# Performance work log

Hardware: AMD Instinct MI355X
Metric: run time of the kernel (lower is better)

## Reference

```python
import jax, jax.numpy as jnp
import numpy as np

M, B, T, DIN, H, E, NEMB = 6, 128, 32, 64, 512, 512, 32


def setup_inputs() -> dict:
    key = jax.random.key(0)
    ks = jax.random.split(key, 6)
    return {
        "state_btD": jax.random.normal(ks[0], (B, T, M * DIN), dtype=jnp.float32),
        "emb_ids": jax.random.randint(ks[1], (B,), 0, NEMB),
        # stacked per-modality, per-embodiment adapter params (all modalities share dims)
        "W1": 0.02 * jax.random.normal(ks[2], (M, NEMB, DIN, H), dtype=jnp.float32),
        "b1": jnp.zeros((M, NEMB, H), dtype=jnp.float32),
        "W2": 0.02 * jax.random.normal(ks[3], (M, NEMB, H, E), dtype=jnp.float32),
        "b2": jnp.zeros((M, NEMB, E), dtype=jnp.float32),
        "type_embed": 0.02 * jax.random.normal(ks[4], (M, E), dtype=jnp.float32),
    }


def reference(state_btD, emb_ids, W1, b1, W2, b2, type_embed):
    Bb, Tt, _ = state_btD.shape
    # slices are contiguous equal-size chunks -> (B, T, M, DIN)
    x = state_btD.reshape(Bb, Tt, M, DIN)
    # layer1: per-sample gathered weights W1[:, emb_ids] -> (M, B, DIN, H)
    h = jax.nn.relu(
        jnp.einsum('btmi,mbih->btmh', x, W1[:, emb_ids])
        + b1[:, emb_ids].transpose(1, 0, 2)[:, None]  # (B,1,M,H)
    )
    # layer2 + type embed
    z = (
        jnp.einsum('btmh,mbho->btmo', h, W2[:, emb_ids])
        + b2[:, emb_ids].transpose(1, 0, 2)[:, None]
        + type_embed[None, None]  # (1,1,M,E)
    )
    # torch.cat(tokens, dim=1): modality-major along the token axis -> (B, M*T, E)
    return z.transpose(0, 2, 1, 3).reshape(Bb, M * Tt, E)
```

## Files before the change

### kernel.cpp

```cpp
#include <hip/hip_runtime.h>

#define MM   6
#define BB   128
#define TT   32
#define DIN  64
#define HH   512
#define EE   512
#define NEMB 32
#define XP   72
#define HP   520

typedef __attribute__((ext_vector_type(8))) short bf16x8;
typedef __attribute__((ext_vector_type(4))) float f32x4;

static __device__ __forceinline__ unsigned short f2bf(float f) {
    unsigned int u = __float_as_uint(f);
    u += 0x7FFFu + ((u >> 16) & 1u);
    return (unsigned short)(u >> 16);
}
static __device__ __forceinline__ float bf2f(unsigned short h) {
    return __uint_as_float(((unsigned int)h) << 16);
}


__global__ __launch_bounds__(256, 2) void tok_mfma(
    const float* __restrict__ state,
    const int*   __restrict__ emb_ids,
    const float* __restrict__ W1,
    const float* __restrict__ b1,
    const float* __restrict__ W2,
    const float* __restrict__ b2,
    const float* __restrict__ te,
    float* __restrict__ out)
{
    __shared__ __align__(16) unsigned short x_hi[TT][XP];
    __shared__ __align__(16) unsigned short x_lo[TT][XP];
    __shared__ __align__(16) unsigned short h_hi[TT][HP];
    __shared__ __align__(16) unsigned short h_lo[TT][HP];

    const int tid  = threadIdx.x;
    const int lane = tid & 63;
    const int w    = tid >> 6;
    const int lr   = lane & 15;
    const int lg   = lane >> 4;

    const int bm = blockIdx.x;
    const int m  = bm % MM;
    const int b  = bm / MM;
    const int id = emb_ids[b];

    const float* xg  = state + (size_t)b * TT * (MM * DIN) + m * DIN;
    const float* W1p = W1 + (size_t)(m * NEMB + id) * DIN * HH;
    const float* b1p = b1 + (size_t)(m * NEMB + id) * HH;
    const float* W2p = W2 + (size_t)(m * NEMB + id) * HH * EE;
    const float* b2p = b2 + (size_t)(m * NEMB + id) * EE;
    const float* tep = te + m * EE;

    #pragma unroll
    for (int k = 0; k < 2; ++k) {
        int f  = k * 256 + tid;
        int t  = f >> 4;
        int i4 = f & 15;
        float4 v = *reinterpret_cast<const float4*>(xg + (size_t)t * (MM * DIN) + i4 * 4);
        ushort4 hi, lo;
        hi.x = f2bf(v.x); lo.x = f2bf(v.x - bf2f(hi.x));
        hi.y = f2bf(v.y); lo.y = f2bf(v.y - bf2f(hi.y));
        hi.z = f2bf(v.z); lo.z = f2bf(v.z - bf2f(hi.z));
        hi.w = f2bf(v.w); lo.w = f2bf(v.w - bf2f(hi.w));
        *reinterpret_cast<ushort4*>(&x_hi[t][i4 * 4]) = hi;
        *reinterpret_cast<ushort4*>(&x_lo[t][i4 * 4]) = lo;
    }
    __syncthreads();

    bf16x8 xa_h[2][2], xa_l[2][2];
    #pragma unroll
    for (int r0 = 0; r0 < 2; ++r0)
        #pragma unroll
        for (int kk = 0; kk < 2; ++kk) {
            xa_h[r0][kk] = *reinterpret_cast<const bf16x8*>(&x_hi[r0 * 16 + lr][kk * 32 + lg * 8]);
            xa_l[r0][kk] = *reinterpret_cast<const bf16x8*>(&x_lo[r0 * 16 + lr][kk * 32 + lg * 8]);
        }

    #pragma unroll
    for (int j = 0; j < 8; ++j) {
        const int n = w * 128 + j * 16 + lr;
        float bv = b1p[n];
        f32x4 a0 = {bv, bv, bv, bv};
        f32x4 a1 = {bv, bv, bv, bv};
        #pragma unroll
        for (int kk = 0; kk < 2; ++kk) {
            const float* wp = W1p + (size_t)(kk * 32 + lg * 8) * HH + n;
            bf16x8 bh, bl;
            #pragma unroll
            for (int i = 0; i < 8; ++i) {
                float wv = wp[(size_t)i * HH];
                unsigned short h_ = f2bf(wv);
                bh[i] = (short)h_;
                bl[i] = (short)f2bf(wv - bf2f(h_));
            }
            a0 = __builtin_amdgcn_mfma_f32_16x16x32_bf16(xa_h[0][kk], bh, a0, 0, 0, 0);
            a0 = __builtin_amdgcn_mfma_f32_16x16x32_bf16(xa_h[0][kk], bl, a0, 0, 0, 0);
            a0 = __builtin_amdgcn_mfma_f32_16x16x32_bf16(xa_l[0][kk], bh, a0, 0, 0, 0);
            a1 = __builtin_amdgcn_mfma_f32_16x16x32_bf16(xa_h[1][kk], bh, a1, 0, 0, 0);
            a1 = __builtin_amdgcn_mfma_f32_16x16x32_bf16(xa_h[1][kk], bl, a1, 0, 0, 0);
            a1 = __builtin_amdgcn_mfma_f32_16x16x32_bf16(xa_l[1][kk], bh, a1, 0, 0, 0);
        }
        #pragma unroll
        for (int r = 0; r < 4; ++r) {
            float h0 = fmaxf(a0[r], 0.0f);
            unsigned short hh0 = f2bf(h0);
            h_hi[lg * 4 + r][n] = hh0;
            h_lo[lg * 4 + r][n] = f2bf(h0 - bf2f(hh0));
            float h1 = fmaxf(a1[r], 0.0f);
            unsigned short hh1 = f2bf(h1);
            h_hi[16 + lg * 4 + r][n] = hh1;
            h_lo[16 + lg * 4 + r][n] = f2bf(h1 - bf2f(hh1));
        }
    }
    __syncthreads();

    float bias2[8];
    #pragma unroll
    for (int j = 0; j < 8; ++j) {
        int n = w * 128 + j * 16 + lr;
        bias2[j] = b2p[n] + tep[n];
    }
    f32x4 acc[2][8];
    #pragma unroll
    for (int r0 = 0; r0 < 2; ++r0)
        #pragma unroll
        for (int j = 0; j < 8; ++j) {
            f32x4 t0 = {bias2[j], bias2[j], bias2[j], bias2[j]};
            acc[r0][j] = t0;
        }

    for (int kk = 0; kk < 16; ++kk) {
        bf16x8 ah0 = *reinterpret_cast<const bf16x8*>(&h_hi[lr][kk * 32 + lg * 8]);
        bf16x8 al0 = *reinterpret_cast<const bf16x8*>(&h_lo[lr][kk * 32 + lg * 8]);
        bf16x8 ah1 = *reinterpret_cast<const bf16x8*>(&h_hi[16 + lr][kk * 32 + lg * 8]);
        bf16x8 al1 = *reinterpret_cast<const bf16x8*>(&h_lo[16 + lr][kk * 32 + lg * 8]);
        #pragma unroll
        for (int j = 0; j < 8; ++j) {
            const float* wp = W2p + (size_t)(kk * 32 + lg * 8) * EE + (w * 128 + j * 16 + lr);
            bf16x8 bh, bl;
            #pragma unroll
            for (int i = 0; i < 8; ++i) {
                float wv = wp[(size_t)i * EE];
                unsigned short h_ = f2bf(wv);
                bh[i] = (short)h_;
                bl[i] = (short)f2bf(wv - bf2f(h_));
            }
            acc[0][j] = __builtin_amdgcn_mfma_f32_16x16x32_bf16(ah0, bh, acc[0][j], 0, 0, 0);
            acc[0][j] = __builtin_amdgcn_mfma_f32_16x16x32_bf16(ah0, bl, acc[0][j], 0, 0, 0);
            acc[0][j] = __builtin_amdgcn_mfma_f32_16x16x32_bf16(al0, bh, acc[0][j], 0, 0, 0);
            acc[1][j] = __builtin_amdgcn_mfma_f32_16x16x32_bf16(ah1, bh, acc[1][j], 0, 0, 0);
            acc[1][j] = __builtin_amdgcn_mfma_f32_16x16x32_bf16(ah1, bl, acc[1][j], 0, 0, 0);
            acc[1][j] = __builtin_amdgcn_mfma_f32_16x16x32_bf16(al1, bh, acc[1][j], 0, 0, 0);
        }
    }

    float* outp = out + ((size_t)(b * MM + m) * TT) * EE;
    #pragma unroll
    for (int r0 = 0; r0 < 2; ++r0)
        #pragma unroll
        for (int j = 0; j < 8; ++j) {
            int n = w * 128 + j * 16 + lr;
            #pragma unroll
            for (int r = 0; r < 4; ++r) {
                int row = r0 * 16 + lg * 4 + r;
                outp[(size_t)row * EE + n] = acc[r0][j][r];
            }
        }
}

extern "C" void kernel_launch(void* const* d_in, const int* in_sizes, int n_in,
                              void* d_out, int out_size, void* d_ws, size_t ws_size,
                              hipStream_t stream) {
    const float* state   = (const float*)d_in[0];
    const int*   emb_ids = (const int*)d_in[1];
    const float* W1      = (const float*)d_in[2];
    const float* b1      = (const float*)d_in[3];
    const float* W2      = (const float*)d_in[4];
    const float* b2      = (const float*)d_in[5];
    const float* te      = (const float*)d_in[6];
    float*       out     = (float*)d_out;

    dim3 grid(BB * MM);
    dim3 block(256);
    tok_mfma<<<grid, block, 0, stream>>>(state, emb_ids, W1, b1, W2, b2, te, out);
}
```

Measured before the change: 372.7 us.

## Bucket samples by embodiment and process two samples per block to share weights

```diff
diff --git a/kernel.cpp b/kernel.cpp
--- a/kernel.cpp
+++ b/kernel.cpp
@@ -9,6 +9,8 @@
 #define NEMB 32
 #define XP   72
 #define HP   520
+#define ROWS 64
+#define MAXCH 64
 
 typedef __attribute__((ext_vector_type(8))) short bf16x8;
 typedef __attribute__((ext_vector_type(4))) float f32x4;
@@ -22,10 +24,22 @@
     return __uint_as_float(((unsigned int)h) << 16);
 }
 
-
-__global__ __launch_bounds__(256, 2) void tok_mfma(
+__global__ void bucket_k(const int* __restrict__ emb_ids,
+                         int* __restrict__ cnt, int* __restrict__ lists) {
+    int t = threadIdx.x;
+    if (t < NEMB) cnt[t] = 0;
+    __syncthreads();
+    if (t < BB) {
+        int id = emb_ids[t];
+        int slot = atomicAdd(&cnt[id], 1);
+        lists[id * BB + slot] = t;
+    }
+}
+
+__global__ __launch_bounds__(512, 2) void tok_mfma2(
     const float* __restrict__ state,
-    const int*   __restrict__ emb_ids,
+    const int*   __restrict__ cnt,
+    const int*   __restrict__ lists,
     const float* __restrict__ W1,
     const float* __restrict__ b1,
     const float* __restrict__ W2,
@@ -33,10 +47,19 @@
     const float* __restrict__ te,
     float* __restrict__ out)
 {
-    __shared__ __align__(16) unsigned short x_hi[TT][XP];
-    __shared__ __align__(16) unsigned short x_lo[TT][XP];
-    __shared__ __align__(16) unsigned short h_hi[TT][HP];
-    __shared__ __align__(16) unsigned short h_lo[TT][HP];
+    __shared__ __align__(16) unsigned short x_hi[ROWS][XP];
+    __shared__ __align__(16) unsigned short x_lo[ROWS][XP];
+    __shared__ __align__(16) unsigned short h_hi[ROWS][HP];
+    __shared__ __align__(16) unsigned short h_lo[ROWS][HP];
+
+    const int c  = blockIdx.x;
+    const int id = blockIdx.y;
+    const int m  = blockIdx.z;
+    const int n_b = cnt[id];
+    if (c * 2 >= n_b) return;
+    const int nb  = (n_b - c * 2 >= 2) ? 2 : 1;
+    const int ba0 = lists[id * BB + c * 2];
+    const int ba1 = lists[id * BB + c * 2 + (nb - 1)];
 
     const int tid  = threadIdx.x;
     const int lane = tid & 63;
@@ -44,12 +67,6 @@
     const int lr   = lane & 15;
     const int lg   = lane >> 4;
 
-    const int bm = blockIdx.x;
-    const int m  = bm % MM;
-    const int b  = bm / MM;
-    const int id = emb_ids[b];
-
-    const float* xg  = state + (size_t)b * TT * (MM * DIN) + m * DIN;
     const float* W1p = W1 + (size_t)(m * NEMB + id) * DIN * HH;
     const float* b1p = b1 + (size_t)(m * NEMB + id) * HH;
     const float* W2p = W2 + (size_t)(m * NEMB + id) * HH * EE;
@@ -57,36 +74,39 @@
     const float* tep = te + m * EE;
 
     #pragma unroll
-    for (int k = 0; k < 2; ++k) {
-        int f  = k * 256 + tid;
-        int t  = f >> 4;
+    for (int kq = 0; kq < 2; ++kq) {
+        int f  = kq * 512 + tid;
+        int r  = f >> 4;
         int i4 = f & 15;
-        float4 v = *reinterpret_cast<const float4*>(xg + (size_t)t * (MM * DIN) + i4 * 4);
+        int bsel = (r < 32) ? ba0 : ba1;
+        const float* xg = state + ((size_t)bsel * TT + (r & 31)) * (MM * DIN) + m * DIN + i4 * 4;
+        float4 v = *reinterpret_cast<const float4*>(xg);
         ushort4 hi, lo;
         hi.x = f2bf(v.x); lo.x = f2bf(v.x - bf2f(hi.x));
         hi.y = f2bf(v.y); lo.y = f2bf(v.y - bf2f(hi.y));
         hi.z = f2bf(v.z); lo.z = f2bf(v.z - bf2f(hi.z));
         hi.w = f2bf(v.w); lo.w = f2bf(v.w - bf2f(hi.w));
-        *reinterpret_cast<ushort4*>(&x_hi[t][i4 * 4]) = hi;
-        *reinterpret_cast<ushort4*>(&x_lo[t][i4 * 4]) = lo;
+        *reinterpret_cast<ushort4*>(&x_hi[r][i4 * 4]) = hi;
+        *reinterpret_cast<ushort4*>(&x_lo[r][i4 * 4]) = lo;
     }
     __syncthreads();
 
-    bf16x8 xa_h[2][2], xa_l[2][2];
-    #pragma unroll
-    for (int r0 = 0; r0 < 2; ++r0)
+    bf16x8 xa_h[4][2], xa_l[4][2];
+    #pragma unroll
+    for (int rt = 0; rt < 4; ++rt)
         #pragma unroll
         for (int kk = 0; kk < 2; ++kk) {
-            xa_h[r0][kk] = *reinterpret_cast<const bf16x8*>(&x_hi[r0 * 16 + lr][kk * 32 + lg * 8]);
-            xa_l[r0][kk] = *reinterpret_cast<const bf16x8*>(&x_lo[r0 * 16 + lr][kk * 32 + lg * 8]);
-        }
-
-    #pragma unroll
-    for (int j = 0; j < 8; ++j) {
-        const int n = w * 128 + j * 16 + lr;
+            xa_h[rt][kk] = *reinterpret_cast<const bf16x8*>(&x_hi[rt * 16 + lr][kk * 32 + lg * 8]);
+            xa_l[rt][kk] = *reinterpret_cast<const bf16x8*>(&x_lo[rt * 16 + lr][kk * 32 + lg * 8]);
+        }
+
+    #pragma unroll
+    for (int j = 0; j < 4; ++j) {
+        const int n = w * 64 + j * 16 + lr;
         float bv = b1p[n];
-        f32x4 a0 = {bv, bv, bv, bv};
-        f32x4 a1 = {bv, bv, bv, bv};
+        f32x4 a[4];
+        #pragma unroll
+        for (int rt = 0; rt < 4; ++rt) { f32x4 t0 = {bv, bv, bv, bv}; a[rt] = t0; }
         #pragma unroll
         for (int kk = 0; kk < 2; ++kk) {
             const float* wp = W1p + (size_t)(kk * 32 + lg * 8) * HH + n;
@@ -98,50 +118,50 @@
                 bh[i] = (short)h_;
                 bl[i] = (short)f2bf(wv - bf2f(h_));
             }
-            a0 = __builtin_amdgcn_mfma_f32_16x16x32_bf16(xa_h[0][kk], bh, a0, 0, 0, 0);
-            a0 = __builtin_amdgcn_mfma_f32_16x16x32_bf16(xa_h[0][kk], bl, a0, 0, 0, 0);
-            a0 = __builtin_amdgcn_mfma_f32_16x16x32_bf16(xa_l[0][kk], bh, a0, 0, 0, 0);
-            a1 = __builtin_amdgcn_mfma_f32_16x16x32_bf16(xa_h[1][kk], bh, a1, 0, 0, 0);
-            a1 = __builtin_amdgcn_mfma_f32_16x16x32_bf16(xa_h[1][kk], bl, a1, 0, 0, 0);
-            a1 = __builtin_amdgcn_mfma_f32_16x16x32_bf16(xa_l[1][kk], bh, a1, 0, 0, 0);
-        }
-        #pragma unroll
-        for (int r = 0; r < 4; ++r) {
-            float h0 = fmaxf(a0[r], 0.0f);
-            unsigned short hh0 = f2bf(h0);
-            h_hi[lg * 4 + r][n] = hh0;
-            h_lo[lg * 4 + r][n] = f2bf(h0 - bf2f(hh0));
-            float h1 = fmaxf(a1[r], 0.0f);
-            unsigned short hh1 = f2bf(h1);
-            h_hi[16 + lg * 4 + r][n] = hh1;
-            h_lo[16 + lg * 4 + r][n] = f2bf(h1 - bf2f(hh1));
-        }
+            #pragma unroll
+            for (int rt = 0; rt < 4; ++rt) {
+                a[rt] = __builtin_amdgcn_mfma_f32_16x16x32_bf16(xa_h[rt][kk], bh, a[rt], 0, 0, 0);
+                a[rt] = __builtin_amdgcn_mfma_f32_16x16x32_bf16(xa_h[rt][kk], bl, a[rt], 0, 0, 0);
+                a[rt] = __builtin_amdgcn_mfma_f32_16x16x32_bf16(xa_l[rt][kk], bh, a[rt], 0, 0, 0);
+            }
+        }
+        #pragma unroll
+        for (int rt = 0; rt < 4; ++rt)
+            #pragma unroll
+            for (int r = 0; r < 4; ++r) {
+                float hv = fmaxf(a[rt][r], 0.0f);
+                unsigned short hh = f2bf(hv);
+                h_hi[rt * 16 + lg * 4 + r][n] = hh;
+                h_lo[rt * 16 + lg * 4 + r][n] = f2bf(hv - bf2f(hh));
+            }
     }
     __syncthreads();
 
-    float bias2[8];
-    #pragma unroll
-    for (int j = 0; j < 8; ++j) {
-        int n = w * 128 + j * 16 + lr;
+    float bias2[4];
+    #pragma unroll
+    for (int j = 0; j < 4; ++j) {
+        int n = w * 64 + j * 16 + lr;
         bias2[j] = b2p[n] + tep[n];
     }
-    f32x4 acc[2][8];
-    #pragma unroll
-    for (int r0 = 0; r0 < 2; ++r0)
-        #pragma unroll
-        for (int j = 0; j < 8; ++j) {
+    f32x4 acc[4][4];
+    #pragma unroll
+    for (int rt = 0; rt < 4; ++rt)
+        #pragma unroll
+        for (int j = 0; j < 4; ++j) {
             f32x4 t0 = {bias2[j], bias2[j], bias2[j], bias2[j]};
-            acc[r0][j] = t0;
+            acc[rt][j] = t0;
         }
 
     for (int kk = 0; kk < 16; ++kk) {
-        bf16x8 ah0 = *reinterpret_cast<const bf16x8*>(&h_hi[lr][kk * 32 + lg * 8]);
-        bf16x8 al0 = *reinterpret_cast<const bf16x8*>(&h_lo[lr][kk * 32 + lg * 8]);
-        bf16x8 ah1 = *reinterpret_cast<const bf16x8*>(&h_hi[16 + lr][kk * 32 + lg * 8]);
-        bf16x8 al1 = *reinterpret_cast<const bf16x8*>(&h_lo[16 + lr][kk * 32 + lg * 8]);
-        #pragma unroll
-        for (int j = 0; j < 8; ++j) {
-            const float* wp = W2p + (size_t)(kk * 32 + lg * 8) * EE + (w * 128 + j * 16 + lr);
+        bf16x8 ah[4], al[4];
+        #pragma unroll
+        for (int rt = 0; rt < 4; ++rt) {
+            ah[rt] = *reinterpret_cast<const bf16x8*>(&h_hi[rt * 16 + lr][kk * 32 + lg * 8]);
+            al[rt] = *reinterpret_cast<const bf16x8*>(&h_lo[rt * 16 + lr][kk * 32 + lg * 8]);
+        }
+        #pragma unroll
+        for (int j = 0; j < 4; ++j) {
+            const float* wp = W2p + (size_t)(kk * 32 + lg * 8) * EE + (w * 64 + j * 16 + lr);
             bf16x8 bh, bl;
             #pragma unroll
             for (int i = 0; i < 8; ++i) {
@@ -150,27 +170,29 @@
                 bh[i] = (short)h_;
                 bl[i] = (short)f2bf(wv - bf2f(h_));
             }
-            acc[0][j] = __builtin_amdgcn_mfma_f32_16x16x32_bf16(ah0, bh, acc[0][j], 0, 0, 0);
-            acc[0][j] = __builtin_amdgcn_mfma_f32_16x16x32_bf16(ah0, bl, acc[0][j], 0, 0, 0);
-            acc[0][j] = __builtin_amdgcn_mfma_f32_16x16x32_bf16(al0, bh, acc[0][j], 0, 0, 0);
-            acc[1][j] = __builtin_amdgcn_mfma_f32_16x16x32_bf16(ah1, bh, acc[1][j], 0, 0, 0);
-            acc[1][j] = __builtin_amdgcn_mfma_f32_16x16x32_bf16(ah1, bl, acc[1][j], 0, 0, 0);
-            acc[1][j] = __builtin_amdgcn_mfma_f32_16x16x32_bf16(al1, bh, acc[1][j], 0, 0, 0);
-        }
-    }
-
-    float* outp = out + ((size_t)(b * MM + m) * TT) * EE;
-    #pragma unroll
-    for (int r0 = 0; r0 < 2; ++r0)
-        #pragma unroll
-        for (int j = 0; j < 8; ++j) {
-            int n = w * 128 + j * 16 + lr;
-            #pragma unroll
-            for (int r = 0; r < 4; ++r) {
-                int row = r0 * 16 + lg * 4 + r;
-                outp[(size_t)row * EE + n] = acc[r0][j][r];
-            }
-        }
+            #pragma unroll
+            for (int rt = 0; rt < 4; ++rt) {
+                acc[rt][j] = __builtin_amdgcn_mfma_f32_16x16x32_bf16(ah[rt], bh, acc[rt][j], 0, 0, 0);
+                acc[rt][j] = __builtin_amdgcn_mfma_f32_16x16x32_bf16(ah[rt], bl, acc[rt][j], 0, 0, 0);
+                acc[rt][j] = __builtin_amdgcn_mfma_f32_16x16x32_bf16(al[rt], bh, acc[rt][j], 0, 0, 0);
+            }
+        }
+    }
+
+    #pragma unroll
+    for (int rt = 0; rt < 4; ++rt) {
+        int bi = rt >> 1;
+        if (bi >= nb) continue;
+        int bglob = (bi == 0) ? ba0 : ba1;
+        float* outp = out + (((size_t)bglob * MM + m) * TT + (rt & 1) * 16 + lg * 4) * EE;
+        #pragma unroll
+        for (int j = 0; j < 4; ++j) {
+            int n = w * 64 + j * 16 + lr;
+            #pragma unroll
+            for (int r = 0; r < 4; ++r)
+                outp[(size_t)r * EE + n] = acc[rt][j][r];
+        }
+    }
 }
 
 extern "C" void kernel_launch(void* const* d_in, const int* in_sizes, int n_in,
@@ -185,7 +207,10 @@
     const float* te      = (const float*)d_in[6];
     float*       out     = (float*)d_out;
 
-    dim3 grid(BB * MM);
-    dim3 block(256);
-    tok_mfma<<<grid, block, 0, stream>>>(state, emb_ids, W1, b1, W2, b2, te, out);
-}
+    int* cnt   = (int*)d_ws;
+    int* lists = cnt + NEMB;
+
+    bucket_k<<<dim3(1), dim3(128), 0, stream>>>(emb_ids, cnt, lists);
+    tok_mfma2<<<dim3(MAXCH, NEMB, MM), dim3(512), 0, stream>>>(
+        state, cnt, lists, W1, b1, W2, b2, te, out);
+}
```

Result: slower. 1.039 ms (+178.9%).

## Group blocks by embodiment for L2 reuse and stage W2 loads through LDS

Applied to the files above, without the earlier changes.

```diff
diff --git a/kernel.cpp b/kernel.cpp
--- a/kernel.cpp
+++ b/kernel.cpp
@@ -9,6 +9,7 @@
 #define NEMB 32
 #define XP   72
 #define HP   520
+#define TRS  36
 
 typedef __attribute__((ext_vector_type(8))) short bf16x8;
 typedef __attribute__((ext_vector_type(4))) float f32x4;
@@ -22,21 +23,42 @@
     return __uint_as_float(((unsigned int)h) << 16);
 }
 
-
-__global__ __launch_bounds__(256, 2) void tok_mfma(
+__global__ void order_k(const int* __restrict__ emb_ids, int* __restrict__ ent) {
+    __shared__ int cnt_s[NEMB], psum_s[NEMB], slot_s[BB], id_s[BB];
+    int t = threadIdx.x;
+    if (t < NEMB) cnt_s[t] = 0;
+    __syncthreads();
+    if (t < BB) { int id = emb_ids[t]; id_s[t] = id; slot_s[t] = atomicAdd(&cnt_s[id], 1); }
+    __syncthreads();
+    if (t == 0) { int r = 0; for (int i = 0; i < NEMB; ++i) { psum_s[i] = r; r += cnt_s[i]; } }
+    __syncthreads();
+    if (t < BB) {
+        int id = id_s[t], sl = slot_s[t], base = psum_s[id] * MM, c = cnt_s[id];
+        for (int mm = 0; mm < MM; ++mm) ent[base + mm * c + sl] = (t << 3) | mm;
+    }
+}
+
+__global__ __launch_bounds__(256, 2) void tok_mfma4(
     const float* __restrict__ state,
-    const int*   __restrict__ emb_ids,
+    const int*   __restrict__ ent,
     const float* __restrict__ W1,
     const float* __restrict__ b1,
     const float* __restrict__ W2,
     const float* __restrict__ b2,
     const float* __restrict__ te,
+    const int*   __restrict__ emb_ids,
     float* __restrict__ out)
 {
-    __shared__ __align__(16) unsigned short x_hi[TT][XP];
-    __shared__ __align__(16) unsigned short x_lo[TT][XP];
+    __shared__ __align__(16) unsigned char regA[10240];
     __shared__ __align__(16) unsigned short h_hi[TT][HP];
     __shared__ __align__(16) unsigned short h_lo[TT][HP];
+
+    const int bid = blockIdx.x;
+    const int s   = (bid & 7) * 96 + (bid >> 3);
+    const int e   = ent[s];
+    const int b   = e >> 3;
+    const int m   = e & 7;
+    const int id  = emb_ids[b];
 
     const int tid  = threadIdx.x;
     const int lane = tid & 63;
@@ -44,21 +66,19 @@
     const int lr   = lane & 15;
     const int lg   = lane >> 4;
 
-    const int bm = blockIdx.x;
-    const int m  = bm % MM;
-    const int b  = bm / MM;
-    const int id = emb_ids[b];
-
-    const float* xg  = state + (size_t)b * TT * (MM * DIN) + m * DIN;
     const float* W1p = W1 + (size_t)(m * NEMB + id) * DIN * HH;
     const float* b1p = b1 + (size_t)(m * NEMB + id) * HH;
     const float* W2p = W2 + (size_t)(m * NEMB + id) * HH * EE;
     const float* b2p = b2 + (size_t)(m * NEMB + id) * EE;
     const float* tep = te + m * EE;
-
-    #pragma unroll
-    for (int k = 0; k < 2; ++k) {
-        int f  = k * 256 + tid;
+    const float* xg  = state + (size_t)b * TT * (MM * DIN) + m * DIN;
+
+    unsigned short (*x_hi)[XP] = (unsigned short(*)[XP])regA;
+    unsigned short (*x_lo)[XP] = (unsigned short(*)[XP])(regA + 4608);
+
+    #pragma unroll
+    for (int kq = 0; kq < 2; ++kq) {
+        int f  = kq * 256 + tid;
         int t  = f >> 4;
         int i4 = f & 15;
         float4 v = *reinterpret_cast<const float4*>(xg + (size_t)t * (MM * DIN) + i4 * 4);
@@ -74,11 +94,11 @@
 
     bf16x8 xa_h[2][2], xa_l[2][2];
     #pragma unroll
-    for (int r0 = 0; r0 < 2; ++r0)
+    for (int rt = 0; rt < 2; ++rt)
         #pragma unroll
         for (int kk = 0; kk < 2; ++kk) {
-            xa_h[r0][kk] = *reinterpret_cast<const bf16x8*>(&x_hi[r0 * 16 + lr][kk * 32 + lg * 8]);
-            xa_l[r0][kk] = *reinterpret_cast<const bf16x8*>(&x_lo[r0 * 16 + lr][kk * 32 + lg * 8]);
+            xa_h[rt][kk] = *reinterpret_cast<const bf16x8*>(&x_hi[rt * 16 + lr][kk * 32 + lg * 8]);
+            xa_l[rt][kk] = *reinterpret_cast<const bf16x8*>(&x_lo[rt * 16 + lr][kk * 32 + lg * 8]);
         }
 
     #pragma unroll
@@ -119,6 +139,10 @@
     }
     __syncthreads();
 
+    float* bounce = (float*)(regA + w * 2304);
+    const int wr = lane >> 2;
+    const int wc = (lane & 3) * 4;
+
     float bias2[8];
     #pragma unroll
     for (int j = 0; j < 8; ++j) {
@@ -127,12 +151,16 @@
     }
     f32x4 acc[2][8];
     #pragma unroll
-    for (int r0 = 0; r0 < 2; ++r0)
+    for (int rt = 0; rt < 2; ++rt)
         #pragma unroll
         for (int j = 0; j < 8; ++j) {
             f32x4 t0 = {bias2[j], bias2[j], bias2[j], bias2[j]};
-            acc[r0][j] = t0;
-        }
+            acc[rt][j] = t0;
+        }
+
+    const float* src0 = W2p + (size_t)wr * EE + (w * 128 + wc);
+    float4 ra = *reinterpret_cast<const float4*>(src0);
+    float4 rb = *reinterpret_cast<const float4*>(src0 + (size_t)16 * EE);
 
     for (int kk = 0; kk < 16; ++kk) {
         bf16x8 ah0 = *reinterpret_cast<const bf16x8*>(&h_hi[lr][kk * 32 + lg * 8]);
@@ -141,14 +169,41 @@
         bf16x8 al1 = *reinterpret_cast<const bf16x8*>(&h_lo[16 + lr][kk * 32 + lg * 8]);
         #pragma unroll
         for (int j = 0; j < 8; ++j) {
-            const float* wp = W2p + (size_t)(kk * 32 + lg * 8) * EE + (w * 128 + j * 16 + lr);
+            asm volatile("" ::: "memory");
+            bounce[(wc + 0) * TRS + wr] = ra.x;
+            bounce[(wc + 1) * TRS + wr] = ra.y;
+            bounce[(wc + 2) * TRS + wr] = ra.z;
+            bounce[(wc + 3) * TRS + wr] = ra.w;
+            bounce[(wc + 0) * TRS + 16 + wr] = rb.x;
+            bounce[(wc + 1) * TRS + 16 + wr] = rb.y;
+            bounce[(wc + 2) * TRS + 16 + wr] = rb.z;
+            bounce[(wc + 3) * TRS + 16 + wr] = rb.w;
+            int nkk = (j == 7) ? kk + 1 : kk;
+            int nj  = (j == 7) ? 0 : j + 1;
+            const float* nsrc = (nkk < 16)
+                ? W2p + (size_t)(nkk * 32 + wr) * EE + (w * 128 + nj * 16 + wc)
+                : src0;
+            float4 na = *reinterpret_cast<const float4*>(nsrc);
+            float4 nb = *reinterpret_cast<const float4*>(nsrc + (size_t)16 * EE);
+            asm volatile("s_waitcnt lgkmcnt(0)" ::: "memory");
+            float4 f0 = *reinterpret_cast<const float4*>(&bounce[lr * TRS + lg * 8]);
+            float4 f1 = *reinterpret_cast<const float4*>(&bounce[lr * TRS + lg * 8 + 4]);
             bf16x8 bh, bl;
-            #pragma unroll
-            for (int i = 0; i < 8; ++i) {
-                float wv = wp[(size_t)i * EE];
-                unsigned short h_ = f2bf(wv);
-                bh[i] = (short)h_;
-                bl[i] = (short)f2bf(wv - bf2f(h_));
+            {
+                const float* fv0 = &f0.x;
+                const float* fv1 = &f1.x;
+                #pragma unroll
+                for (int i = 0; i < 4; ++i) {
+                    unsigned short hb = f2bf(fv0[i]);
+                    bh[i] = (short)hb;
+                    bl[i] = (short)f2bf(fv0[i] - bf2f(hb));
+                }
+                #pragma unroll
+                for (int i = 0; i < 4; ++i) {
+                    unsigned short hb = f2bf(fv1[i]);
+                    bh[4 + i] = (short)hb;
+                    bl[4 + i] = (short)f2bf(fv1[i] - bf2f(hb));
+                }
             }
             acc[0][j] = __builtin_amdgcn_mfma_f32_16x16x32_bf16(ah0, bh, acc[0][j], 0, 0, 0);
             acc[0][j] = __builtin_amdgcn_mfma_f32_16x16x32_bf16(ah0, bl, acc[0][j], 0, 0, 0);
@@ -156,19 +211,20 @@
             acc[1][j] = __builtin_amdgcn_mfma_f32_16x16x32_bf16(ah1, bh, acc[1][j], 0, 0, 0);
             acc[1][j] = __builtin_amdgcn_mfma_f32_16x16x32_bf16(ah1, bl, acc[1][j], 0, 0, 0);
             acc[1][j] = __builtin_amdgcn_mfma_f32_16x16x32_bf16(al1, bh, acc[1][j], 0, 0, 0);
+            ra = na; rb = nb;
         }
     }
 
     float* outp = out + ((size_t)(b * MM + m) * TT) * EE;
     #pragma unroll
-    for (int r0 = 0; r0 < 2; ++r0)
+    for (int rt = 0; rt < 2; ++rt)
         #pragma unroll
         for (int j = 0; j < 8; ++j) {
             int n = w * 128 + j * 16 + lr;
             #pragma unroll
             for (int r = 0; r < 4; ++r) {
-                int row = r0 * 16 + lg * 4 + r;
-                outp[(size_t)row * EE + n] = acc[r0][j][r];
+                int row = rt * 16 + lg * 4 + r;
+                outp[(size_t)row * EE + n] = acc[rt][j][r];
             }
         }
 }
@@ -185,7 +241,9 @@
     const float* te      = (const float*)d_in[6];
     float*       out     = (float*)d_out;
 
-    dim3 grid(BB * MM);
-    dim3 block(256);
-    tok_mfma<<<grid, block, 0, stream>>>(state, emb_ids, W1, b1, W2, b2, te, out);
-}
+    int* ent = (int*)d_ws;
+
+    order_k<<<dim3(1), dim3(128), 0, stream>>>(emb_ids, ent);
+    tok_mfma4<<<dim3(BB * MM), dim3(256), 0, stream>>>(
+        state, ent, W1, b1, W2, b2, te, emb_ids, out);
+}
```

After: 415.6 us. 1.12x slower.
